# Optimization experiments

Measured on AMD Instinct MI355X. Metric: run time of the kernel, lower is better.

Reference implementation:

```python
import jax, jax.numpy as jnp
import numpy as np

N_HEAD = 16

def setup_inputs() -> dict:
    key = jax.random.key(0)
    k1, k2, k3 = jax.random.split(key, 3)
    B, S, D = 4, 2048, 1024
    x = jax.random.normal(k1, (B, S, D), dtype=jnp.float32)
    w_attn = jax.random.normal(k2, (D, 3 * D), dtype=jnp.float32) * 0.02
    b_attn = jnp.zeros((3 * D,), dtype=jnp.float32)
    w_proj = jax.random.normal(k3, (D, D), dtype=jnp.float32) * 0.02
    b_proj = jnp.zeros((D,), dtype=jnp.float32)
    return {"x": x, "w_attn": w_attn, "b_attn": b_attn, "w_proj": w_proj, "b_proj": b_proj}

def reference(x, w_attn, b_attn, w_proj, b_proj):
    B, S, D = x.shape
    H = N_HEAD
    dh = D // H
    # c_attn (fan_in_fan_out Conv1D-style: y = x @ W + b)
    qkv = x @ w_attn + b_attn                      # [B,S,3D]
    q, k, v = jnp.split(qkv, 3, axis=-1)
    q = q.reshape(B, S, H, dh).transpose(0, 2, 1, 3)   # [B,H,S,dh]
    k = k.reshape(B, S, H, dh).transpose(0, 2, 3, 1)   # [B,H,dh,S]  (split_heads k=True)
    v = v.reshape(B, S, H, dh).transpose(0, 2, 1, 3)   # [B,H,S,dh]
    # scores = Q K^T, scaled by sqrt(d_head) since scale=True
    w = jnp.einsum('bhid,bhdj->bhij', q, k) / jnp.sqrt(jnp.asarray(dh, x.dtype))
    # causal mask blending exactly as original: w*b - 1e10*(1-b)
    b = jnp.tril(jnp.ones((S, S), dtype=x.dtype))[None, None]
    w = w * b - 1e10 * (1.0 - b)
    w = jax.nn.softmax(w, axis=-1)
    a = jnp.einsum('bhij,bhjd->bhid', w, v)        # [B,H,S,dh]
    a = a.transpose(0, 2, 1, 3).reshape(B, S, D)   # merge_heads
    out = a @ w_proj + b_proj                      # c_proj
    present = jnp.stack((k.transpose(0, 1, 3, 2), v))  # [2,B,H,S,dh]
    return out, present
```

## Files before the change

### kernel.cpp

```cpp
#include <hip/hip_runtime.h>
#include <stdint.h>

typedef unsigned short u16;
typedef __attribute__((ext_vector_type(8))) __bf16 bf16x8;
typedef __attribute__((ext_vector_type(4))) __bf16 bf16x4v;
typedef __attribute__((ext_vector_type(4))) float f32x4;
typedef __attribute__((ext_vector_type(4))) unsigned short u16x4;
typedef __attribute__((ext_vector_type(8))) unsigned short u16x8;

#define MFMA16(a,b,c) __builtin_amdgcn_mfma_f32_16x16x32_bf16(a,b,c,0,0,0)

static __device__ __forceinline__ float fexp2(float x){
#if __has_builtin(__builtin_amdgcn_exp2f)
  return __builtin_amdgcn_exp2f(x);
#else
  float r; asm("v_exp_f32 %0, %1" : "=v"(r) : "v"(x)); return r;
#endif
}

static __device__ __forceinline__ u16 f2b(float f){
  uint32_t u = __float_as_uint(f);
  u += 0x7fffu + ((u >> 16) & 1u);
  return (u16)(u >> 16);
}

static __device__ __forceinline__ void gload_lds16(const void* g, void* l){
  __builtin_amdgcn_global_load_lds(
      (__attribute__((address_space(1))) void*)(uintptr_t)g,
      (__attribute__((address_space(3))) void*)(uintptr_t)l,
      16, 0, 0);
}

__global__ __launch_bounds__(256) void cvt_bf16(const float* __restrict__ in,
                                                u16* __restrict__ out, int n){
  int i = (blockIdx.x * 256 + threadIdx.x) * 4;
  if (i >= n) return;
  float4 v = *(const float4*)(in + i);
  u16x4 o;
  o.x = f2b(v.x); o.y = f2b(v.y); o.z = f2b(v.z); o.w = f2b(v.w);
  *(u16x4*)(out + i) = o;
}

__global__ __launch_bounds__(256) void transpose_cvt(const float* __restrict__ in,
                                                     u16* __restrict__ out,
                                                     int K, int N){
  __shared__ float tile[32][33];
  const int nb = blockIdx.x * 32, kb = blockIdx.y * 32;
  const int tx = threadIdx.x, ty = threadIdx.y;
#pragma unroll
  for (int i = 0; i < 32; i += 8)
    tile[ty + i][tx] = in[(size_t)(kb + ty + i) * N + nb + tx];
  __syncthreads();
#pragma unroll
  for (int i = 0; i < 32; i += 8)
    out[(size_t)(nb + ty + i) * K + kb + tx] = f2b(tile[tx][ty + i]);
}

template<int MODE>
__global__ __launch_bounds__(512, 2) void gemm_pipe(
    const u16* __restrict__ A, const u16* __restrict__ Bt,
    const float* __restrict__ bias, float* __restrict__ Cout,
    u16* __restrict__ q_bf, u16* __restrict__ k_bf, u16* __restrict__ vT_bf,
    int N, int K)
{
  extern __shared__ u16 smem[];
  const int nT = K >> 5;
  const int tid = threadIdx.x;
  const int w = tid >> 6, lane = tid & 63;
  const int l15 = lane & 15, lhi = lane >> 4;
  const int wr = w >> 1, wc = w & 1;
  const int mBase = blockIdx.y * 256, nBase = blockIdx.x * 128;

  const int r0 = tid >> 2;
  const int ch = (tid & 3) ^ (r0 & 3);
  const u16* Ag  = A  + (size_t)(mBase + r0) * K + ch * 8;
  const u16* Ag2 = Ag + (size_t)128 * K;
  const u16* Bg  = Bt + (size_t)(nBase + r0) * K + ch * 8;

  f32x4 acc[4][4];
#pragma unroll
  for (int i = 0; i < 4; ++i)
#pragma unroll
    for (int j = 0; j < 4; ++j) acc[i][j] = f32x4{0.f, 0.f, 0.f, 0.f};

  auto stage = [&](int kt){
    char* buf = (char*)smem + (kt % 3) * 24576;
    const int kb = kt << 5;
    gload_lds16(Ag  + kb, buf + tid * 16);
    gload_lds16(Ag2 + kb, buf + 8192 + tid * 16);
    gload_lds16(Bg  + kb, buf + 16384 + tid * 16);
  };

  stage(0); stage(1);

  for (int kt = 0; kt < nT; ++kt){
    if (kt == nT - 1) asm volatile("s_waitcnt vmcnt(0)" ::: "memory");
    else              asm volatile("s_waitcnt vmcnt(3)" ::: "memory");
    __builtin_amdgcn_s_barrier();
    const char* Ab = (const char*)smem + (kt % 3) * 24576;
    const char* Bb = Ab + 16384;
#define LDT(base, row) (*(const bf16x8*)((base) + ((row) << 6) + (((lhi ^ ((row) & 3))) << 4)))
    bf16x8 a0, a1, a2, a3, b0, b1, b2, b3;
    {
      const int ar = wr * 64 + l15;
      a0 = LDT(Ab, ar); a1 = LDT(Ab, ar + 16); a2 = LDT(Ab, ar + 32); a3 = LDT(Ab, ar + 48);
      const int br = wc * 64 + l15;
      b0 = LDT(Bb, br); b1 = LDT(Bb, br + 16); b2 = LDT(Bb, br + 32); b3 = LDT(Bb, br + 48);
    }
#undef LDT
    if (kt + 2 < nT) stage(kt + 2);
    __builtin_amdgcn_s_setprio(1);
    acc[0][0] = MFMA16(a0, b0, acc[0][0]); acc[0][1] = MFMA16(a0, b1, acc[0][1]);
    acc[0][2] = MFMA16(a0, b2, acc[0][2]); acc[0][3] = MFMA16(a0, b3, acc[0][3]);
    acc[1][0] = MFMA16(a1, b0, acc[1][0]); acc[1][1] = MFMA16(a1, b1, acc[1][1]);
    acc[1][2] = MFMA16(a1, b2, acc[1][2]); acc[1][3] = MFMA16(a1, b3, acc[1][3]);
    acc[2][0] = MFMA16(a2, b0, acc[2][0]); acc[2][1] = MFMA16(a2, b1, acc[2][1]);
    acc[2][2] = MFMA16(a2, b2, acc[2][2]); acc[2][3] = MFMA16(a2, b3, acc[2][3]);
    acc[3][0] = MFMA16(a3, b0, acc[3][0]); acc[3][1] = MFMA16(a3, b1, acc[3][1]);
    acc[3][2] = MFMA16(a3, b2, acc[3][2]); acc[3][3] = MFMA16(a3, b3, acc[3][3]);
    __builtin_amdgcn_s_setprio(0);
  }

  if (MODE == 0){
#pragma unroll
    for (int ni = 0; ni < 4; ++ni){
      const int col = nBase + wc * 64 + ni * 16 + l15;
      const float bv = bias[col];
#pragma unroll
      for (int mi = 0; mi < 4; ++mi)
#pragma unroll
        for (int r = 0; r < 4; ++r){
          const int row = mBase + wr * 64 + mi * 16 + lhi * 4 + r;
          Cout[(size_t)row * N + col] = acc[mi][ni][r] + bv;
        }
    }
    return;
  }

  const int sec = nBase >> 10;
  const int nn0 = nBase & 1023;
  const int bb_ = mBase >> 11;
  const int s0  = mBase & 2047;

  if (sec == 2){
#pragma unroll
    for (int ni = 0; ni < 4; ++ni){
      const int c = wc * 64 + ni * 16 + l15;
      const int nn = nn0 + c;
      const int h = nn >> 6, d = nn & 63;
      const float bv = bias[nBase + c];
#pragma unroll
      for (int mi = 0; mi < 4; ++mi){
        const int sb = s0 + wr * 64 + mi * 16 + lhi * 4;
        u16x4 pk;
#pragma unroll
        for (int r = 0; r < 4; ++r){
          const float v = acc[mi][ni][r] + bv;
          pk[r] = f2b(v);
          Cout[16777216 + ((size_t)(bb_ * 16 + h) * 2048 + sb + r) * 64 + d] = v;
        }
        *(u16x4*)(vT_bf + ((size_t)(bb_ * 16 + h) * 64 + d) * 2048 + sb) = pk;
      }
    }
    return;
  }

  __syncthreads();
  const float qscl = (sec == 0) ? 0.1803368801111204f : 1.0f;
#pragma unroll
  for (int ni = 0; ni < 4; ++ni){
    const int c = wc * 64 + ni * 16 + l15;
    const float bv = bias[nBase + c];
#pragma unroll
    for (int mi = 0; mi < 4; ++mi)
#pragma unroll
      for (int r = 0; r < 4; ++r){
        const int rl = wr * 64 + mi * 16 + lhi * 4 + r;
        smem[rl * 128 + (c ^ ((rl & 7) << 3))] = f2b((acc[mi][ni][r] + bv) * qscl);
      }
  }
  if (sec == 1){
#pragma unroll
    for (int ni = 0; ni < 4; ++ni){
      const int c = wc * 64 + ni * 16 + l15;
      const int nn = nn0 + c;
      const int h = nn >> 6, d = nn & 63;
      const float bv = bias[nBase + c];
#pragma unroll
      for (int mi = 0; mi < 4; ++mi)
#pragma unroll
        for (int r = 0; r < 4; ++r){
          const int s = s0 + wr * 64 + mi * 16 + lhi * 4 + r;
          Cout[8388608 + ((size_t)(bb_ * 16 + h) * 2048 + s) * 64 + d] = acc[mi][ni][r] + bv;
        }
    }
  }
  __syncthreads();
  {
    const int row = tid >> 1, half = tid & 1;
    u16* base = (sec == 0 ? q_bf : k_bf);
#pragma unroll
    for (int i = 0; i < 8; ++i){
      const int c0 = half * 64 + i * 8;
      const int h = (nn0 >> 6) + (c0 >> 6);
      u16x8 vv = *(const u16x8*)&smem[row * 128 + (c0 ^ ((row & 7) << 3))];
      *(u16x8*)(base + ((size_t)(bb_ * 16 + h) * 2048 + s0 + row) * 64 + (c0 & 63)) = vv;
    }
  }
}

__global__ __launch_bounds__(256) void attn_kern(
    const u16* __restrict__ q_bf, const u16* __restrict__ k_bf,
    const u16* __restrict__ vT_bf, u16* __restrict__ a_bf)
{
  const int S = 2048;
  const int id = (int)blockIdx.x + 8 * (int)blockIdx.y;
  const int xcd = id & 7, j = id >> 3;
  const int bh = xcd + 8 * (j & 7);
  const int bx = j >> 3;

  const int tid = threadIdx.x, w = tid >> 6, lane = tid & 63;
  const int l15 = lane & 15, lhi = lane >> 4;
  const u16* qp = q_bf + (size_t)bh * S * 64;
  const char* kbytes = (const char*)(k_bf + (size_t)bh * S * 64);
  const char* vbytes = (const char*)(vT_bf + (size_t)bh * 64 * S);
  const int b = bh >> 4, h = bh & 15;

  __shared__ u16 Kbuf[2][64 * 64];
  __shared__ u16 Vbuf[2][64 * 64];
  __shared__ u16 P_all[4][32 * 64];
  char* Pc = (char*)&P_all[w][0];
  const int swz = (l15 & 7) << 4;

  const int srow = tid >> 3;
  const int sch  = (tid & 7) ^ (srow & 7);

  auto process = [&](f32x4 (&s)[4], float &m, float &l, f32x4 (&o)[4],
                     const bf16x8 (&vf)[8], int qr0g, bool domask, int jb, int gofs){
    if (domask){
      const int q = qr0g + l15;
#pragma unroll
      for (int nf = 0; nf < 4; ++nf)
#pragma unroll
        for (int r = 0; r < 4; ++r){
          const int kv = jb + nf * 16 + lhi * 4 + r;
          if (kv > q) s[nf][r] = -1e10f;
        }
    }
    float a0 = fmaxf(s[0][0], s[0][1]), a1 = fmaxf(s[0][2], s[0][3]);
    float a2 = fmaxf(s[1][0], s[1][1]), a3 = fmaxf(s[1][2], s[1][3]);
    float a4 = fmaxf(s[2][0], s[2][1]), a5 = fmaxf(s[2][2], s[2][3]);
    float a6 = fmaxf(s[3][0], s[3][1]), a7 = fmaxf(s[3][2], s[3][3]);
    float x = fmaxf(fmaxf(fmaxf(a0,a1), fmaxf(a2,a3)),
                    fmaxf(fmaxf(a4,a5), fmaxf(a6,a7)));
    x = fmaxf(x, __shfl_xor(x, 16));
    x = fmaxf(x, __shfl_xor(x, 32));
    if (__any(x - m > 8.0f)){
      const float mn = fmaxf(m, x);
      const float sc = fexp2(m - mn);
      m = mn;
      l *= sc;
      float scq[4];
#pragma unroll
      for (int r = 0; r < 4; ++r)
        scq[r] = __shfl(sc, (lane & 48) | (lhi * 4 + r));
#pragma unroll
      for (int df = 0; df < 4; ++df)
#pragma unroll
        for (int r = 0; r < 4; ++r) o[df][r] *= scq[r];
    }
    float p[16];
#pragma unroll
    for (int nf = 0; nf < 4; ++nf)
#pragma unroll
      for (int r = 0; r < 4; ++r) p[nf*4+r] = fexp2(s[nf][r] - m);
    float rs = (((p[0]+p[1])+(p[2]+p[3])) + ((p[4]+p[5])+(p[6]+p[7])))
             + (((p[8]+p[9])+(p[10]+p[11])) + ((p[12]+p[13])+(p[14]+p[15])));
    rs += __shfl_xor(rs, 16);
    rs += __shfl_xor(rs, 32);
    l += rs;
#pragma unroll
    for (int nf = 0; nf < 4; ++nf){
      bf16x4v pk;
#pragma unroll
      for (int r = 0; r < 4; ++r) pk[r] = (__bf16)p[nf*4+r];
      *(bf16x4v*)(Pc + gofs + ((l15 * 128 + nf * 32 + lhi * 8) ^ swz)) = pk;
    }
    __builtin_amdgcn_s_setprio(1);
#pragma unroll
    for (int kk = 0; kk < 2; ++kk){
      const bf16x8 pa = *(const bf16x8*)(Pc + gofs + ((l15 * 128 + kk * 64 + lhi * 16) ^ swz));
#pragma unroll
      for (int df = 0; df < 4; ++df)
        o[df] = MFMA16(pa, vf[kk*4+df], o[df]);
    }
    __builtin_amdgcn_s_setprio(0);
  };

  for (int half = 0; half < 2; ++half){
    const int qt = (half == 0) ? (15 - bx) : bx;
    const int qr0 = qt * 128 + w * 32;

    bf16x8 qf[2][2];
#pragma unroll
    for (int g = 0; g < 2; ++g){
      qf[g][0] = *(const bf16x8*)&qp[(qr0 + g * 16 + l15) * 64 + lhi * 8];
      qf[g][1] = *(const bf16x8*)&qp[(qr0 + g * 16 + l15) * 64 + 32 + lhi * 8];
    }

    f32x4 o[2][4];
#pragma unroll
    for (int g = 0; g < 2; ++g)
#pragma unroll
      for (int df = 0; df < 4; ++df) o[g][df] = f32x4{0.f,0.f,0.f,0.f};
    float m[2] = {-1e30f, -1e30f}, l[2] = {0.f, 0.f};

    const int nStage = 2 * qt + 2;
    const int nC = 2 * qt + 1 + (w >> 1);
    int cur = 0;

    gload_lds16(kbytes + (size_t)srow * 128 + sch * 16,        (char*)Kbuf[0] + w * 1024);
    gload_lds16(kbytes + (size_t)(srow + 32) * 128 + sch * 16, (char*)Kbuf[0] + 4096 + w * 1024);
    gload_lds16(vbytes + (size_t)srow * 4096 + sch * 16,        (char*)Vbuf[0] + w * 1024);
    gload_lds16(vbytes + (size_t)(srow + 32) * 4096 + sch * 16, (char*)Vbuf[0] + 4096 + w * 1024);
    __syncthreads();

    for (int it = 0; it < nStage; ++it){
      const int jb = it * 64;
      if (it + 1 < nStage){
        const char* kb2 = kbytes + (size_t)(jb + 64) * 128;
        const char* vb2 = vbytes + (size_t)(jb + 64) * 2;
        char* kd = (char*)Kbuf[cur ^ 1];
        char* vd = (char*)Vbuf[cur ^ 1];
        gload_lds16(kb2 + (size_t)srow * 128 + sch * 16,        kd + w * 1024);
        gload_lds16(kb2 + (size_t)(srow + 32) * 128 + sch * 16, kd + 4096 + w * 1024);
        gload_lds16(vb2 + (size_t)srow * 4096 + sch * 16,        vd + w * 1024);
        gload_lds16(vb2 + (size_t)(srow + 32) * 4096 + sch * 16, vd + 4096 + w * 1024);
      }
      if (it < nC){
        const char* Kc = (const char*)Kbuf[cur];
        const char* Vc = (const char*)Vbuf[cur];
        bf16x8 kf[8];
#pragma unroll
        for (int nf = 0; nf < 4; ++nf)
#pragma unroll
          for (int kk = 0; kk < 2; ++kk)
            kf[2*nf+kk] = *(const bf16x8*)(Kc + (((nf * 16 + l15) * 128 + kk * 64 + lhi * 16) ^ swz));
        f32x4 s[2][4];
        __builtin_amdgcn_s_setprio(1);
#pragma unroll
        for (int g = 0; g < 2; ++g)
#pragma unroll
          for (int nf = 0; nf < 4; ++nf){
            f32x4 z = {0.f, 0.f, 0.f, 0.f};
            z = MFMA16(kf[2*nf], qf[g][0], z);
            z = MFMA16(kf[2*nf+1], qf[g][1], z);
            s[g][nf] = z;
          }
        __builtin_amdgcn_s_setprio(0);
        bf16x8 vf[8];
#pragma unroll
        for (int kk = 0; kk < 2; ++kk)
#pragma unroll
          for (int df = 0; df < 4; ++df)
            vf[kk*4+df] = *(const bf16x8*)(Vc + (((df * 16 + l15) * 128 + kk * 64 + lhi * 16) ^ swz));
        const bool domask = (it == nC - 1);
        process(s[0], m[0], l[0], o[0], vf, qr0,      domask, jb, 0);
        process(s[1], m[1], l[1], o[1], vf, qr0 + 16, domask, jb, 2048);
      }
      __syncthreads();
      cur ^= 1;
    }

#pragma unroll
    for (int g = 0; g < 2; ++g){
      const float linv = 1.0f / l[g];
      float lr[4];
#pragma unroll
      for (int r = 0; r < 4; ++r)
        lr[r] = __shfl(linv, (lane & 48) | (lhi * 4 + r));
#pragma unroll
      for (int r = 0; r < 4; ++r){
        const int qrow = qr0 + g * 16 + lhi * 4 + r;
#pragma unroll
        for (int df = 0; df < 4; ++df)
          a_bf[((size_t)b * 2048 + qrow) * 1024 + h * 64 + df * 16 + l15] = f2b(o[g][df][r] * lr[r]);
      }
    }
  }
}

extern "C" void kernel_launch(void* const* d_in, const int* in_sizes, int n_in,
                              void* d_out, int out_size, void* d_ws, size_t ws_size,
                              hipStream_t stream)
{
  const float* x      = (const float*)d_in[0];
  const float* w_attn = (const float*)d_in[1];
  const float* b_attn = (const float*)d_in[2];
  const float* w_proj = (const float*)d_in[3];
  const float* b_proj = (const float*)d_in[4];
  float* out = (float*)d_out;
  char* ws = (char*)d_ws;
  const size_t MB = 1u << 20;
  u16* x_bf  = (u16*)(ws + 0);
  u16* wA_T  = (u16*)(ws + 16 * MB);
  u16* wP_T  = (u16*)(ws + 22 * MB);
  u16* q_bf  = (u16*)(ws + 24 * MB);
  u16* k_bf  = (u16*)(ws + 40 * MB);
  u16* vT_bf = (u16*)(ws + 56 * MB);
  u16* a_bf  = x_bf;

  cvt_bf16<<<dim3(8192), dim3(256), 0, stream>>>(x, x_bf, 4 * 2048 * 1024);
  transpose_cvt<<<dim3(96, 32), dim3(32, 8), 0, stream>>>(w_attn, wA_T, 1024, 3072);
  transpose_cvt<<<dim3(32, 32), dim3(32, 8), 0, stream>>>(w_proj, wP_T, 1024, 1024);
  gemm_pipe<1><<<dim3(24, 32), dim3(512), 73728, stream>>>(
      x_bf, wA_T, b_attn, out, q_bf, k_bf, vT_bf, 3072, 1024);
  attn_kern<<<dim3(8, 64), dim3(256), 0, stream>>>(q_bf, k_bf, vT_bf, a_bf);
  gemm_pipe<0><<<dim3(8, 32), dim3(512), 73728, stream>>>(
      a_bf, wP_T, b_proj, out, nullptr, nullptr, nullptr, 1024, 1024);
}
```

Before: 194.3 us.

## Pair mirrored 64-row query tiles in one causal K/V sweep per block

The attention kernel now gives each block two 64-row query tiles, one early and one late (tA=31-bx, tB=bx). Both tiles are processed in a single pass over the shared K/V stream, so each loaded K/V chunk is reused by both tiles until the shorter causal range ends. Previously each block ran two separate sequential sweeps over 128-row tiles. The grid doubles to 1024 blocks with a launch-bounds occupancy hint of 4, and per-wave P scratch in LDS shrinks, aiming for better load balance and occupancy at the cost of less per-wave work and smaller MFMA batches.

Result: slower. 289.0 us (+48.8%).

```diff
diff --git a/kernel.cpp b/kernel.cpp
--- a/kernel.cpp
+++ b/kernel.cpp
@@ -209,12 +209,12 @@
   }
 }
 
-__global__ __launch_bounds__(256) void attn_kern(
+__global__ __launch_bounds__(256, 4) void attn_kern(
     const u16* __restrict__ q_bf, const u16* __restrict__ k_bf,
     const u16* __restrict__ vT_bf, u16* __restrict__ a_bf)
 {
   const int S = 2048;
-  const int id = (int)blockIdx.x + 8 * (int)blockIdx.y;
+  const int id = (int)blockIdx.x + 16 * (int)blockIdx.y;
   const int xcd = id & 7, j = id >> 3;
   const int bh = xcd + 8 * (j & 7);
   const int bx = j >> 3;
@@ -228,15 +228,32 @@
 
   __shared__ u16 Kbuf[2][64 * 64];
   __shared__ u16 Vbuf[2][64 * 64];
-  __shared__ u16 P_all[4][32 * 64];
+  __shared__ u16 P_all[4][16 * 64];
   char* Pc = (char*)&P_all[w][0];
   const int swz = (l15 & 7) << 4;
 
   const int srow = tid >> 3;
   const int sch  = (tid & 7) ^ (srow & 7);
 
+  const int tA = 31 - bx, tB = bx;
+  const int qr0A = tA * 64 + w * 16;
+  const int qr0B = tB * 64 + w * 16;
+  const int nStage = tA + 1;
+  const int nCB    = tB + 1;
+
+  bf16x8 qfA[2], qfB[2];
+  qfA[0] = *(const bf16x8*)&qp[(qr0A + l15) * 64 + lhi * 8];
+  qfA[1] = *(const bf16x8*)&qp[(qr0A + l15) * 64 + 32 + lhi * 8];
+  qfB[0] = *(const bf16x8*)&qp[(qr0B + l15) * 64 + lhi * 8];
+  qfB[1] = *(const bf16x8*)&qp[(qr0B + l15) * 64 + 32 + lhi * 8];
+
+  f32x4 oA[4], oB[4];
+#pragma unroll
+  for (int df = 0; df < 4; ++df){ oA[df] = f32x4{0.f,0.f,0.f,0.f}; oB[df] = f32x4{0.f,0.f,0.f,0.f}; }
+  float mA = -1e30f, lA = 0.f, mB = -1e30f, lB = 0.f;
+
   auto process = [&](f32x4 (&s)[4], float &m, float &l, f32x4 (&o)[4],
-                     const bf16x8 (&vf)[8], int qr0g, bool domask, int jb, int gofs){
+                     const bf16x8 (&vf)[8], int qr0g, bool domask, int jb){
     if (domask){
       const int q = qr0g + l15;
 #pragma unroll
@@ -284,12 +301,12 @@
       bf16x4v pk;
 #pragma unroll
       for (int r = 0; r < 4; ++r) pk[r] = (__bf16)p[nf*4+r];
-      *(bf16x4v*)(Pc + gofs + ((l15 * 128 + nf * 32 + lhi * 8) ^ swz)) = pk;
+      *(bf16x4v*)(Pc + ((l15 * 128 + nf * 32 + lhi * 8) ^ swz)) = pk;
     }
     __builtin_amdgcn_s_setprio(1);
 #pragma unroll
     for (int kk = 0; kk < 2; ++kk){
-      const bf16x8 pa = *(const bf16x8*)(Pc + gofs + ((l15 * 128 + kk * 64 + lhi * 16) ^ swz));
+      const bf16x8 pa = *(const bf16x8*)(Pc + ((l15 * 128 + kk * 64 + lhi * 16) ^ swz));
 #pragma unroll
       for (int df = 0; df < 4; ++df)
         o[df] = MFMA16(pa, vf[kk*4+df], o[df]);
@@ -297,97 +314,84 @@
     __builtin_amdgcn_s_setprio(0);
   };
 
-  for (int half = 0; half < 2; ++half){
-    const int qt = (half == 0) ? (15 - bx) : bx;
-    const int qr0 = qt * 128 + w * 32;
-
-    bf16x8 qf[2][2];
-#pragma unroll
-    for (int g = 0; g < 2; ++g){
-      qf[g][0] = *(const bf16x8*)&qp[(qr0 + g * 16 + l15) * 64 + lhi * 8];
-      qf[g][1] = *(const bf16x8*)&qp[(qr0 + g * 16 + l15) * 64 + 32 + lhi * 8];
-    }
-
-    f32x4 o[2][4];
-#pragma unroll
-    for (int g = 0; g < 2; ++g)
-#pragma unroll
-      for (int df = 0; df < 4; ++df) o[g][df] = f32x4{0.f,0.f,0.f,0.f};
-    float m[2] = {-1e30f, -1e30f}, l[2] = {0.f, 0.f};
-
-    const int nStage = 2 * qt + 2;
-    const int nC = 2 * qt + 1 + (w >> 1);
-    int cur = 0;
-
-    gload_lds16(kbytes + (size_t)srow * 128 + sch * 16,        (char*)Kbuf[0] + w * 1024);
-    gload_lds16(kbytes + (size_t)(srow + 32) * 128 + sch * 16, (char*)Kbuf[0] + 4096 + w * 1024);
-    gload_lds16(vbytes + (size_t)srow * 4096 + sch * 16,        (char*)Vbuf[0] + w * 1024);
-    gload_lds16(vbytes + (size_t)(srow + 32) * 4096 + sch * 16, (char*)Vbuf[0] + 4096 + w * 1024);
+  int cur = 0;
+  gload_lds16(kbytes + (size_t)srow * 128 + sch * 16,        (char*)Kbuf[0] + w * 1024);
+  gload_lds16(kbytes + (size_t)(srow + 32) * 128 + sch * 16, (char*)Kbuf[0] + 4096 + w * 1024);
+  gload_lds16(vbytes + (size_t)srow * 4096 + sch * 16,        (char*)Vbuf[0] + w * 1024);
+  gload_lds16(vbytes + (size_t)(srow + 32) * 4096 + sch * 16, (char*)Vbuf[0] + 4096 + w * 1024);
+  __syncthreads();
+
+  for (int it = 0; it < nStage; ++it){
+    const int jb = it * 64;
+    if (it + 1 < nStage){
+      const char* kb2 = kbytes + (size_t)(jb + 64) * 128;
+      const char* vb2 = vbytes + (size_t)(jb + 64) * 2;
+      char* kd = (char*)Kbuf[cur ^ 1];
+      char* vd = (char*)Vbuf[cur ^ 1];
+      gload_lds16(kb2 + (size_t)srow * 128 + sch * 16,        kd + w * 1024);
+      gload_lds16(kb2 + (size_t)(srow + 32) * 128 + sch * 16, kd + 4096 + w * 1024);
+      gload_lds16(vb2 + (size_t)srow * 4096 + sch * 16,        vd + w * 1024);
+      gload_lds16(vb2 + (size_t)(srow + 32) * 4096 + sch * 16, vd + 4096 + w * 1024);
+    }
+    {
+      const char* Kc = (const char*)Kbuf[cur];
+      const char* Vc = (const char*)Vbuf[cur];
+      const bool doB = (it < nCB);
+      bf16x8 kf[8];
+#pragma unroll
+      for (int nf = 0; nf < 4; ++nf)
+#pragma unroll
+        for (int kk = 0; kk < 2; ++kk)
+          kf[2*nf+kk] = *(const bf16x8*)(Kc + (((nf * 16 + l15) * 128 + kk * 64 + lhi * 16) ^ swz));
+      f32x4 sA[4], sB[4];
+      __builtin_amdgcn_s_setprio(1);
+#pragma unroll
+      for (int nf = 0; nf < 4; ++nf){
+        f32x4 z = {0.f, 0.f, 0.f, 0.f};
+        z = MFMA16(kf[2*nf], qfA[0], z);
+        z = MFMA16(kf[2*nf+1], qfA[1], z);
+        sA[nf] = z;
+      }
+      if (doB){
+#pragma unroll
+        for (int nf = 0; nf < 4; ++nf){
+          f32x4 z = {0.f, 0.f, 0.f, 0.f};
+          z = MFMA16(kf[2*nf], qfB[0], z);
+          z = MFMA16(kf[2*nf+1], qfB[1], z);
+          sB[nf] = z;
+        }
+      }
+      __builtin_amdgcn_s_setprio(0);
+      bf16x8 vf[8];
+#pragma unroll
+      for (int kk = 0; kk < 2; ++kk)
+#pragma unroll
+        for (int df = 0; df < 4; ++df)
+          vf[kk*4+df] = *(const bf16x8*)(Vc + (((df * 16 + l15) * 128 + kk * 64 + lhi * 16) ^ swz));
+      process(sA, mA, lA, oA, vf, qr0A, it == nStage - 1, jb);
+      if (doB)
+        process(sB, mB, lB, oB, vf, qr0B, it == nCB - 1, jb);
+    }
     __syncthreads();
-
-    for (int it = 0; it < nStage; ++it){
-      const int jb = it * 64;
-      if (it + 1 < nStage){
-        const char* kb2 = kbytes + (size_t)(jb + 64) * 128;
-        const char* vb2 = vbytes + (size_t)(jb + 64) * 2;
-        char* kd = (char*)Kbuf[cur ^ 1];
-        char* vd = (char*)Vbuf[cur ^ 1];
-        gload_lds16(kb2 + (size_t)srow * 128 + sch * 16,        kd + w * 1024);
-        gload_lds16(kb2 + (size_t)(srow + 32) * 128 + sch * 16, kd + 4096 + w * 1024);
-        gload_lds16(vb2 + (size_t)srow * 4096 + sch * 16,        vd + w * 1024);
-        gload_lds16(vb2 + (size_t)(srow + 32) * 4096 + sch * 16, vd + 4096 + w * 1024);
-      }
-      if (it < nC){
-        const char* Kc = (const char*)Kbuf[cur];
-        const char* Vc = (const char*)Vbuf[cur];
-        bf16x8 kf[8];
-#pragma unroll
-        for (int nf = 0; nf < 4; ++nf)
-#pragma unroll
-          for (int kk = 0; kk < 2; ++kk)
-            kf[2*nf+kk] = *(const bf16x8*)(Kc + (((nf * 16 + l15) * 128 + kk * 64 + lhi * 16) ^ swz));
-        f32x4 s[2][4];
-        __builtin_amdgcn_s_setprio(1);
-#pragma unroll
-        for (int g = 0; g < 2; ++g)
-#pragma unroll
-          for (int nf = 0; nf < 4; ++nf){
-            f32x4 z = {0.f, 0.f, 0.f, 0.f};
-            z = MFMA16(kf[2*nf], qf[g][0], z);
-            z = MFMA16(kf[2*nf+1], qf[g][1], z);
-            s[g][nf] = z;
-          }
-        __builtin_amdgcn_s_setprio(0);
-        bf16x8 vf[8];
-#pragma unroll
-        for (int kk = 0; kk < 2; ++kk)
-#pragma unroll
-          for (int df = 0; df < 4; ++df)
-            vf[kk*4+df] = *(const bf16x8*)(Vc + (((df * 16 + l15) * 128 + kk * 64 + lhi * 16) ^ swz));
-        const bool domask = (it == nC - 1);
-        process(s[0], m[0], l[0], o[0], vf, qr0,      domask, jb, 0);
-        process(s[1], m[1], l[1], o[1], vf, qr0 + 16, domask, jb, 2048);
-      }
-      __syncthreads();
-      cur ^= 1;
-    }
-
-#pragma unroll
-    for (int g = 0; g < 2; ++g){
-      const float linv = 1.0f / l[g];
-      float lr[4];
-#pragma unroll
-      for (int r = 0; r < 4; ++r)
-        lr[r] = __shfl(linv, (lane & 48) | (lhi * 4 + r));
-#pragma unroll
-      for (int r = 0; r < 4; ++r){
-        const int qrow = qr0 + g * 16 + lhi * 4 + r;
-#pragma unroll
-        for (int df = 0; df < 4; ++df)
-          a_bf[((size_t)b * 2048 + qrow) * 1024 + h * 64 + df * 16 + l15] = f2b(o[g][df][r] * lr[r]);
-      }
-    }
-  }
+    cur ^= 1;
+  }
+
+  auto finalize = [&](float l, f32x4 (&o)[4], int qr0g){
+    const float linv = 1.0f / l;
+    float lr[4];
+#pragma unroll
+    for (int r = 0; r < 4; ++r)
+      lr[r] = __shfl(linv, (lane & 48) | (lhi * 4 + r));
+#pragma unroll
+    for (int r = 0; r < 4; ++r){
+      const int qrow = qr0g + lhi * 4 + r;
+#pragma unroll
+      for (int df = 0; df < 4; ++df)
+        a_bf[((size_t)b * 2048 + qrow) * 1024 + h * 64 + df * 16 + l15] = f2b(o[df][r] * lr[r]);
+    }
+  };
+  finalize(lA, oA, qr0A);
+  finalize(lB, oB, qr0B);
 }
 
 extern "C" void kernel_launch(void* const* d_in, const int* in_sizes, int n_in,
@@ -415,7 +419,7 @@
   transpose_cvt<<<dim3(32, 32), dim3(32, 8), 0, stream>>>(w_proj, wP_T, 1024, 1024);
   gemm_pipe<1><<<dim3(24, 32), dim3(512), 73728, stream>>>(
       x_bf, wA_T, b_attn, out, q_bf, k_bf, vT_bf, 3072, 1024);
-  attn_kern<<<dim3(8, 64), dim3(256), 0, stream>>>(q_bf, k_bf, vT_bf, a_bf);
+  attn_kern<<<dim3(16, 64), dim3(256), 0, stream>>>(q_bf, k_bf, vT_bf, a_bf);
   gemm_pipe<0><<<dim3(8, 32), dim3(512), 73728, stream>>>(
       a_bf, wP_T, b_proj, out, nullptr, nullptr, nullptr, 1024, 1024);
 }
```
